# Performance work log

Hardware: AMD Instinct MI355X
Metric: run time of the kernel (lower is better)

## Reference

```python
import jax, jax.numpy as jnp
import numpy as np

LEVEL = 256
GROUPS = 1
SHIFT = (LEVEL - 1) / 2.0  # symmetric affine shift folded from quant.shift buffer


def qdq(x, clip_val, level=LEVEL, groups=GROUPS, shift=SHIFT):
    """Per-group clip + level quantize-dequantize (what custom_quant.Quant saves/restores).
    clip_val: [groups]. Group split is over equal contiguous chunks of the flattened tensor."""
    shp = x.shape
    xg = x.reshape(groups, -1)
    scale = (2.0 * clip_val) / (level - 1)          # [groups]
    scale = scale.reshape(groups, 1)
    q = jnp.clip(jnp.round(xg / scale + shift), 0.0, level - 1.0)
    return ((q - shift) * scale).reshape(shp)


def setup_inputs() -> dict:
    key = jax.random.key(0)
    k1, k2 = jax.random.split(key)
    # attention-style batched matmul: [B,H,S,Dh] @ [B,H,Dh,S]
    x1 = jax.random.normal(k1, (2, 12, 1024, 64), dtype=jnp.float32)
    x2 = jax.random.normal(k2, (2, 12, 64, 1024), dtype=jnp.float32)
    clip_val1 = 2.0 * jnp.ones((GROUPS,), dtype=jnp.float32)
    clip_val2 = 2.0 * jnp.ones((GROUPS,), dtype=jnp.float32)
    return {"x1": x1, "x2": x2, "clip_val1": clip_val1, "clip_val2": clip_val2}


def reference(x1, x2, clip_val1, clip_val2):
    # Faithful to matmul.forward: the quantized copies are only SAVED for backward;
    # the forward output itself is computed on the full-precision operands.
    # (qdq is exercised in the fwdbwd reference.)
    return jnp.matmul(x1, x2)  # [2,12,1024,1024]
```

## Files before the change

kernel.cpp:

```cpp
#include <hip/hip_runtime.h>
#include <hip/hip_bf16.h>


#define NN 1024
#define KK 64

typedef __attribute__((ext_vector_type(4))) float  float4v;
typedef __attribute__((ext_vector_type(8))) short  bf16x8;
typedef __attribute__((ext_vector_type(16))) float floatx16;

__device__ __forceinline__ short f2bs(float f) {
    union { float f; unsigned u; } in;
    in.f = f;
    unsigned u = in.u;
    return (short)((u + 0x7FFFu + ((u >> 16) & 1u)) >> 16);
}


__global__ __launch_bounds__(256) void reformat_AB(const float* __restrict__ A,
                                                   const float* __restrict__ B,
                                                   short* __restrict__ Aw,
                                                   short* __restrict__ Bw) {
    if (blockIdx.x < 192) {
        int t0 = blockIdx.x * 256 + threadIdx.x;
        #pragma unroll
        for (int it = 0; it < 4; ++it) {
            int task = t0 + it * 49152;
            int bh   = task >> 13;
            int rem  = task & 8191;
            int m    = rem >> 3;
            int kg   = rem & 7;
            const float4v* p = (const float4v*)(A + (size_t)task * 8);
            float4v v0 = p[0];
            float4v v1 = p[1];
            int ks = kg >> 1, q = kg & 1;
            int mt = m >> 5;
            int lane = (m & 31) + (q << 5);
            size_t dst = ((size_t)((bh * 32 + mt) * 4 + ks)) * 512 + (size_t)lane * 8;
            bf16x8 o;
            o[0] = f2bs(v0.x); o[1] = f2bs(v0.y); o[2] = f2bs(v0.z); o[3] = f2bs(v0.w);
            o[4] = f2bs(v1.x); o[5] = f2bs(v1.y); o[6] = f2bs(v1.z); o[7] = f2bs(v1.w);
            *(bf16x8*)(Aw + dst) = o;
        }
    } else {
        int t0 = (blockIdx.x - 192) * 256 + threadIdx.x;
        #pragma unroll
        for (int it = 0; it < 4; ++it) {
            int task = t0 + it * 49152;
            int kg   = task / 24576;
            int rem  = task - kg * 24576;
            int bh   = rem >> 10;
            int n    = rem & 1023;
            const float* p = B + (size_t)bh * 65536 + (size_t)kg * 8192 + n;
            float v0 = p[0 * 1024], v1 = p[1 * 1024], v2 = p[2 * 1024], v3 = p[3 * 1024];
            float v4 = p[4 * 1024], v5 = p[5 * 1024], v6 = p[6 * 1024], v7 = p[7 * 1024];
            int ks = kg >> 1, q = kg & 1;
            int nt = n >> 5;
            int lane = (n & 31) + (q << 5);
            size_t dst = ((size_t)((bh * 32 + nt) * 4 + ks)) * 512 + (size_t)lane * 8;
            bf16x8 o;
            o[0] = f2bs(v0); o[1] = f2bs(v1); o[2] = f2bs(v2); o[3] = f2bs(v3);
            o[4] = f2bs(v4); o[5] = f2bs(v5); o[6] = f2bs(v6); o[7] = f2bs(v7);
            *(bf16x8*)(Bw + dst) = o;
        }
    }
}

__global__ __launch_bounds__(256) void bmm_frag(const short* __restrict__ Aw,
                                                const short* __restrict__ Bw,
                                                float* __restrict__ C) {
    const int tid  = threadIdx.x;
    const int lane = tid & 63;
    const int w    = tid >> 6;
    const int bx = blockIdx.x;
    const int by = blockIdx.y;
    const int bh = blockIdx.z;
    const int wm = (w >> 1) * 2;
    const int wn = (w & 1) * 2;

    const short* Ab = Aw + ((size_t)((bh * 32 + by * 4 + wm) * 4)) * 512 + (size_t)lane * 8;
    const short* Bb = Bw + ((size_t)((bh * 32 + bx * 4 + wn) * 4)) * 512 + (size_t)lane * 8;

    floatx16 acc[2][2];
    #pragma unroll
    for (int mi = 0; mi < 2; ++mi)
        #pragma unroll
        for (int ni = 0; ni < 2; ++ni)
            #pragma unroll
            for (int r = 0; r < 16; ++r)
                acc[mi][ni][r] = 0.0f;

    #pragma unroll
    for (int ks = 0; ks < 4; ++ks) {
        bf16x8 a0 = *(const bf16x8*)(Ab + ks * 512);
        bf16x8 a1 = *(const bf16x8*)(Ab + 2048 + ks * 512);
        bf16x8 b0 = *(const bf16x8*)(Bb + ks * 512);
        bf16x8 b1 = *(const bf16x8*)(Bb + 2048 + ks * 512);
        acc[0][0] = __builtin_amdgcn_mfma_f32_32x32x16_bf16(a0, b0, acc[0][0], 0, 0, 0);
        acc[0][1] = __builtin_amdgcn_mfma_f32_32x32x16_bf16(a0, b1, acc[0][1], 0, 0, 0);
        acc[1][0] = __builtin_amdgcn_mfma_f32_32x32x16_bf16(a1, b0, acc[1][0], 0, 0, 0);
        acc[1][1] = __builtin_amdgcn_mfma_f32_32x32x16_bf16(a1, b1, acc[1][1], 0, 0, 0);
    }

    const int nc    = lane & 31;
    const int rbase = (lane >> 5) * 4;
    float* Cb = C + ((size_t)bh << 20)
                  + (size_t)(by * 128 + wm * 32) * NN
                  + bx * 128 + wn * 32 + nc;

    #pragma unroll
    for (int mi = 0; mi < 2; ++mi) {
        #pragma unroll
        for (int ni = 0; ni < 2; ++ni) {
            float* Ct = Cb + (size_t)(mi * 32) * NN + ni * 32;
            #pragma unroll
            for (int r = 0; r < 16; ++r) {
                int row = rbase + (r & 3) + ((r >> 2) * 8);
                __builtin_nontemporal_store(acc[mi][ni][r], Ct + (size_t)row * NN);
            }
        }
    }
}

extern "C" void kernel_launch(void* const* d_in, const int* in_sizes, int n_in,
                              void* d_out, int out_size, void* d_ws, size_t ws_size,
                              hipStream_t stream) {
    const float* x1 = (const float*)d_in[0];
    const float* x2 = (const float*)d_in[1];
    float* out = (float*)d_out;

    short* Aw = (short*)d_ws;
    short* Bw = Aw + 1572864;

    hipLaunchKernelGGL(reformat_AB, dim3(384), dim3(256), 0, stream, x1, x2, Aw, Bw);
    hipLaunchKernelGGL(bmm_frag, dim3(8, 8, 24), dim3(256), 0, stream, Aw, Bw, out);
}
```

Measured before the change: 123.3 us.

## Fuse bf16 conversion into batched matmul and stage output through LDS for vector stores

Drops the separate reformat kernel. The matmul kernel now reads fp32 A and B straight from global memory and converts them to bf16 in registers just before the MFMA. The epilogue also changes: accumulators are transposed through shared memory so each lane writes 16-byte nontemporal vector stores instead of scalar strided stores. This removes a kernel launch and the workspace round trip, but adds redundant fp32 loads and conversions across blocks, strided scalar B loads, and extra barriers in the epilogue.

```diff
diff --git a/kernel.cpp b/kernel.cpp
--- a/kernel.cpp
+++ b/kernel.cpp
@@ -3,7 +3,6 @@
 
 
 #define NN 1024
-#define KK 64
 
 typedef __attribute__((ext_vector_type(4))) float  float4v;
 typedef __attribute__((ext_vector_type(8))) short  bf16x8;
@@ -16,59 +15,11 @@
     return (short)((u + 0x7FFFu + ((u >> 16) & 1u)) >> 16);
 }
 
+__global__ __launch_bounds__(256) void bmm_fused(const float* __restrict__ A,
+                                                 const float* __restrict__ B,
+                                                 float* __restrict__ C) {
+    __shared__ __align__(16) float tr[4][1024];
 
-__global__ __launch_bounds__(256) void reformat_AB(const float* __restrict__ A,
-                                                   const float* __restrict__ B,
-                                                   short* __restrict__ Aw,
-                                                   short* __restrict__ Bw) {
-    if (blockIdx.x < 192) {
-        int t0 = blockIdx.x * 256 + threadIdx.x;
-        #pragma unroll
-        for (int it = 0; it < 4; ++it) {
-            int task = t0 + it * 49152;
-            int bh   = task >> 13;
-            int rem  = task & 8191;
-            int m    = rem >> 3;
-            int kg   = rem & 7;
-            const float4v* p = (const float4v*)(A + (size_t)task * 8);
-            float4v v0 = p[0];
-            float4v v1 = p[1];
-            int ks = kg >> 1, q = kg & 1;
-            int mt = m >> 5;
-            int lane = (m & 31) + (q << 5);
-            size_t dst = ((size_t)((bh * 32 + mt) * 4 + ks)) * 512 + (size_t)lane * 8;
-            bf16x8 o;
-            o[0] = f2bs(v0.x); o[1] = f2bs(v0.y); o[2] = f2bs(v0.z); o[3] = f2bs(v0.w);
-            o[4] = f2bs(v1.x); o[5] = f2bs(v1.y); o[6] = f2bs(v1.z); o[7] = f2bs(v1.w);
-            *(bf16x8*)(Aw + dst) = o;
-        }
-    } else {
-        int t0 = (blockIdx.x - 192) * 256 + threadIdx.x;
-        #pragma unroll
-        for (int it = 0; it < 4; ++it) {
-            int task = t0 + it * 49152;
-            int kg   = task / 24576;
-            int rem  = task - kg * 24576;
-            int bh   = rem >> 10;
-            int n    = rem & 1023;
-            const float* p = B + (size_t)bh * 65536 + (size_t)kg * 8192 + n;
-            float v0 = p[0 * 1024], v1 = p[1 * 1024], v2 = p[2 * 1024], v3 = p[3 * 1024];
-            float v4 = p[4 * 1024], v5 = p[5 * 1024], v6 = p[6 * 1024], v7 = p[7 * 1024];
-            int ks = kg >> 1, q = kg & 1;
-            int nt = n >> 5;
-            int lane = (n & 31) + (q << 5);
-            size_t dst = ((size_t)((bh * 32 + nt) * 4 + ks)) * 512 + (size_t)lane * 8;
-            bf16x8 o;
-            o[0] = f2bs(v0); o[1] = f2bs(v1); o[2] = f2bs(v2); o[3] = f2bs(v3);
-            o[4] = f2bs(v4); o[5] = f2bs(v5); o[6] = f2bs(v6); o[7] = f2bs(v7);
-            *(bf16x8*)(Bw + dst) = o;
-        }
-    }
-}
-
-__global__ __launch_bounds__(256) void bmm_frag(const short* __restrict__ Aw,
-                                                const short* __restrict__ Bw,
-                                                float* __restrict__ C) {
     const int tid  = threadIdx.x;
     const int lane = tid & 63;
     const int w    = tid >> 6;
@@ -77,9 +28,11 @@
     const int bh = blockIdx.z;
     const int wm = (w >> 1) * 2;
     const int wn = (w & 1) * 2;
+    const int lid = lane & 31;
+    const int q   = lane >> 5;
 
-    const short* Ab = Aw + ((size_t)((bh * 32 + by * 4 + wm) * 4)) * 512 + (size_t)lane * 8;
-    const short* Bb = Bw + ((size_t)((bh * 32 + bx * 4 + wn) * 4)) * 512 + (size_t)lane * 8;
+    const float* Abase = A + (size_t)bh * 65536;
+    const float* Bbase = B + (size_t)bh * 65536;
 
     floatx16 acc[2][2];
     #pragma unroll
@@ -90,33 +43,57 @@
             for (int r = 0; r < 16; ++r)
                 acc[mi][ni][r] = 0.0f;
 
+    const float* pa0 = Abase + (size_t)(by * 128 + (wm + 0) * 32 + lid) * 64 + q * 8;
+    const float* pa1 = Abase + (size_t)(by * 128 + (wm + 1) * 32 + lid) * 64 + q * 8;
+    const int n0 = bx * 128 + (wn + 0) * 32 + lid;
+    const int n1 = bx * 128 + (wn + 1) * 32 + lid;
+
     #pragma unroll
     for (int ks = 0; ks < 4; ++ks) {
-        bf16x8 a0 = *(const bf16x8*)(Ab + ks * 512);
-        bf16x8 a1 = *(const bf16x8*)(Ab + 2048 + ks * 512);
-        bf16x8 b0 = *(const bf16x8*)(Bb + ks * 512);
-        bf16x8 b1 = *(const bf16x8*)(Bb + 2048 + ks * 512);
+        float4v a0lo = *(const float4v*)(pa0 + ks * 16);
+        float4v a0hi = *(const float4v*)(pa0 + ks * 16 + 4);
+        float4v a1lo = *(const float4v*)(pa1 + ks * 16);
+        float4v a1hi = *(const float4v*)(pa1 + ks * 16 + 4);
+        const float* pb0 = Bbase + (size_t)(ks * 16 + q * 8) * NN + n0;
+        const float* pb1 = Bbase + (size_t)(ks * 16 + q * 8) * NN + n1;
+
+        bf16x8 a0, a1, b0, b1;
+        a0[0]=f2bs(a0lo.x); a0[1]=f2bs(a0lo.y); a0[2]=f2bs(a0lo.z); a0[3]=f2bs(a0lo.w);
+        a0[4]=f2bs(a0hi.x); a0[5]=f2bs(a0hi.y); a0[6]=f2bs(a0hi.z); a0[7]=f2bs(a0hi.w);
+        a1[0]=f2bs(a1lo.x); a1[1]=f2bs(a1lo.y); a1[2]=f2bs(a1lo.z); a1[3]=f2bs(a1lo.w);
+        a1[4]=f2bs(a1hi.x); a1[5]=f2bs(a1hi.y); a1[6]=f2bs(a1hi.z); a1[7]=f2bs(a1hi.w);
+        #pragma unroll
+        for (int j = 0; j < 8; ++j) b0[j] = f2bs(pb0[(size_t)j * NN]);
+        #pragma unroll
+        for (int j = 0; j < 8; ++j) b1[j] = f2bs(pb1[(size_t)j * NN]);
+
         acc[0][0] = __builtin_amdgcn_mfma_f32_32x32x16_bf16(a0, b0, acc[0][0], 0, 0, 0);
         acc[0][1] = __builtin_amdgcn_mfma_f32_32x32x16_bf16(a0, b1, acc[0][1], 0, 0, 0);
         acc[1][0] = __builtin_amdgcn_mfma_f32_32x32x16_bf16(a1, b0, acc[1][0], 0, 0, 0);
         acc[1][1] = __builtin_amdgcn_mfma_f32_32x32x16_bf16(a1, b1, acc[1][1], 0, 0, 0);
     }
 
-    const int nc    = lane & 31;
-    const int rbase = (lane >> 5) * 4;
-    float* Cb = C + ((size_t)bh << 20)
-                  + (size_t)(by * 128 + wm * 32) * NN
-                  + bx * 128 + wn * 32 + nc;
-
+    const int rbase = q * 4;
     #pragma unroll
     for (int mi = 0; mi < 2; ++mi) {
         #pragma unroll
         for (int ni = 0; ni < 2; ++ni) {
-            float* Ct = Cb + (size_t)(mi * 32) * NN + ni * 32;
+            __syncthreads();
             #pragma unroll
             for (int r = 0; r < 16; ++r) {
-                int row = rbase + (r & 3) + ((r >> 2) * 8);
-                __builtin_nontemporal_store(acc[mi][ni][r], Ct + (size_t)row * NN);
+                int row = rbase + (r & 3) + (r >> 2) * 8;
+                tr[w][row * 32 + lid] = acc[mi][ni][r];
+            }
+            __syncthreads();
+            float* Ct = C + ((size_t)bh << 20)
+                          + (size_t)(by * 128 + (wm + mi) * 32) * NN
+                          + bx * 128 + (wn + ni) * 32;
+            #pragma unroll
+            for (int g = 0; g < 4; ++g) {
+                float4v v = *(const float4v*)&tr[w][g * 256 + lane * 4];
+                int row = g * 8 + (lane >> 3);
+                __builtin_nontemporal_store(
+                    v, (float4v*)(Ct + (size_t)row * NN + (lane & 7) * 4));
             }
         }
     }
@@ -128,10 +105,7 @@
     const float* x1 = (const float*)d_in[0];
     const float* x2 = (const float*)d_in[1];
     float* out = (float*)d_out;
+    (void)d_ws; (void)ws_size; (void)in_sizes; (void)n_in; (void)out_size;
 
-    short* Aw = (short*)d_ws;
-    short* Bw = Aw + 1572864;
-
-    hipLaunchKernelGGL(reformat_AB, dim3(384), dim3(256), 0, stream, x1, x2, Aw, Bw);
-    hipLaunchKernelGGL(bmm_frag, dim3(8, 8, 24), dim3(256), 0, stream, Aw, Bw, out);
+    hipLaunchKernelGGL(bmm_fused, dim3(8, 8, 24), dim3(256), 0, stream, x1, x2, out);
 }
```

After: 135.8 us. 1.1x slower.
